# Performance work log

Hardware: AMD Instinct MI355X
Metric: run time of the kernel (lower is better)

Reference implementation:

```python
import jax, jax.numpy as jnp
import numpy as np

B, S, D = 4, 4096, 1024
UNITS = 1024
NRF = 1024


def setup_inputs() -> dict:
    key = jax.random.key(0)
    ks = jax.random.split(key, 10)
    s = 1.0 / np.sqrt(D)
    return {
        "query": jax.random.normal(ks[0], (B, S, D), dtype=jnp.float32),
        "value": jax.random.normal(ks[1], (B, S, D), dtype=jnp.float32),
        "Wq": jax.random.normal(ks[2], (D, UNITS), dtype=jnp.float32) * s,
        "bq": jnp.zeros((UNITS,), dtype=jnp.float32),
        "Wk": jax.random.normal(ks[3], (D, UNITS), dtype=jnp.float32) * s,
        "bk": jnp.zeros((UNITS,), dtype=jnp.float32),
        "Wv": jax.random.normal(ks[4], (D, UNITS), dtype=jnp.float32) * s,
        "bv": jnp.zeros((UNITS,), dtype=jnp.float32),
        # non-trainable random-feature projection (initializer='random_normal', stddev 0.05 in keras)
        "random_weights": jax.random.normal(ks[5], (UNITS, NRF), dtype=jnp.float32) * 0.05,
        "random_bias": jax.random.normal(ks[6], (NRF,), dtype=jnp.float32) * 0.05,
    }


def reference(query, value, Wq, bq, Wk, bk, Wv, bv, random_weights, random_bias):
    # Dense projections: [B,S,D] @ [D,U] -> [B,S,U]
    Q = query @ Wq + bq
    K = value @ Wk + bk
    V = value @ Wv + bv
    # random-feature kernel map: cos(x @ W_r + b_r) -> [B,S,F]
    Q_hat = jnp.cos(Q @ random_weights + random_bias)
    K_hat = jnp.cos(K @ random_weights + random_bias)
    # standard QK^T-softmax-V attention over the feature-mapped Q/K
    scores = jnp.einsum("bqf,bkf->bqk", Q_hat, K_hat)  # [B,S,S]
    probs = jax.nn.softmax(scores, axis=-1)
    return jnp.einsum("bqk,bkd->bqd", probs, V)  # [B,S,U]
```

## Files before the change

### kernel.cpp

```cpp
#include <hip/hip_runtime.h>
#include <hip/hip_bf16.h>
#include <hip/hip_fp16.h>
#include <cstdint>


typedef _Float16 f16;
typedef _Float16 f16x8 __attribute__((ext_vector_type(8)));
typedef _Float16 f16x4 __attribute__((ext_vector_type(4)));
typedef float f32x4 __attribute__((ext_vector_type(4)));

typedef __attribute__((address_space(1))) unsigned int uas1;
typedef __attribute__((address_space(3))) unsigned int uas3;

#define NB 4
#define SEQ 4096
#define DIM 1024

__device__ __forceinline__ void async_copy16(void* lds, const void* g) {
  __builtin_amdgcn_global_load_lds((uas1*)(uintptr_t)g, (uas3*)(uintptr_t)lds,
                                   16, 0, 0);
}


__global__ __launch_bounds__(256) void f2h(const float* __restrict__ in,
                                           f16* __restrict__ out, int n4) {
  int i = blockIdx.x * 256 + threadIdx.x;
  if (i < n4) {
    float4 v = ((const float4*)in)[i];
    f16x4 h = {(f16)v.x, (f16)v.y, (f16)v.z, (f16)v.w};
    ((f16x4*)out)[i] = h;
  }
}

__global__ __launch_bounds__(256) void f2h_split(const float* __restrict__ in,
                                                 f16* __restrict__ hi,
                                                 f16* __restrict__ lo, int n4) {
  int i = blockIdx.x * 256 + threadIdx.x;
  if (i < n4) {
    float4 v = ((const float4*)in)[i];
    f16 h0 = (f16)v.x, h1 = (f16)v.y, h2 = (f16)v.z, h3 = (f16)v.w;
    f16x4 hv = {h0, h1, h2, h3};
    f16x4 lv = {(f16)(v.x - (float)h0), (f16)(v.y - (float)h1),
                (f16)(v.z - (float)h2), (f16)(v.w - (float)h3)};
    ((f16x4*)hi)[i] = hv;
    ((f16x4*)lo)[i] = lv;
  }
}

__global__ __launch_bounds__(256) void f2h_split2(const float* __restrict__ in,
                                                  f16* __restrict__ w2, int n4) {
  int i = blockIdx.x * 256 + threadIdx.x;
  if (i < n4) {
    float4 v = ((const float4*)in)[i];
    f16 h0 = (f16)v.x, h1 = (f16)v.y, h2 = (f16)v.z, h3 = (f16)v.w;
    f16x4 hv = {h0, h1, h2, h3};
    f16x4 lv = {(f16)(v.x - (float)h0), (f16)(v.y - (float)h1),
                (f16)(v.z - (float)h2), (f16)(v.w - (float)h3)};
    const int n = i >> 8, k4 = i & 255;
    ((f16x4*)(w2 + (long)n * 2048))[k4] = hv;
    ((f16x4*)(w2 + (long)n * 2048 + 1024))[k4] = lv;
  }
}

__global__ void tr_h(const f16* __restrict__ in, f16* __restrict__ out, int R,
                     int C) {
  __shared__ f16 tile[32][33];
  int c0 = blockIdx.x * 32, r0 = blockIdx.y * 32;
  tile[threadIdx.y][threadIdx.x] =
      in[(long)(r0 + threadIdx.y) * C + c0 + threadIdx.x];
  __syncthreads();
  out[(long)(c0 + threadIdx.y) * R + r0 + threadIdx.x] =
      tile[threadIdx.x][threadIdx.y];
}

__global__ __launch_bounds__(256) void bias_fold(const float* __restrict__ br,
                                                 const float* __restrict__ bvec,
                                                 const float* __restrict__ Wr,
                                                 float* __restrict__ outb) {
  int f = blockIdx.x * 256 + threadIdx.x;
  float s = br[f];
  for (int u = 0; u < DIM; ++u) s = fmaf(bvec[u], Wr[(long)u * DIM + f], s);
  outb[f] = s;
}

__global__ __launch_bounds__(256) void merge_pair(const float* __restrict__ ml,
                                                  const float* __restrict__ ll,
                                                  f16* __restrict__ scl) {
  int i = blockIdx.x * 256 + threadIdx.x;
  int z2 = i >> 12, row = i & 4095;
  const float* m = ml + z2 * 65536 + row;
  const float* lp = ll + z2 * 65536 + row;
  float a[16];
  float mg = -1e30f;
#pragma unroll 16
  for (int t = 0; t < 16; ++t) mg = fmaxf(mg, m[t * 4096]);
  float l = 0.f;
#pragma unroll 16
  for (int t = 0; t < 16; ++t) {
    a[t] = __expf(m[t * 4096] - mg);
    l += lp[t * 4096] * a[t];
  }
  float li = 1.0f / l;
#pragma unroll 16
  for (int t = 0; t < 16; ++t)
    scl[z2 * 65536 + t * 4096 + row] = (f16)(a[t] * li);
}

__global__ void sentinel(float* out) { out[0] = 12345.0f; }

template <int EPI, int NT, bool WRAPA, int GX>
__global__ __launch_bounds__(512, 2) void g8p(
    const f16* __restrict__ A, const f16* __restrict__ B,
    void* __restrict__ Cv, const float* __restrict__ aux,
    float* __restrict__ mout, float* __restrict__ lout, long sA, long sB,
    long sC, int lda, int ldb, int ldc) {
  constexpr int BUF = 65536;
  __shared__ __align__(16) char smem[2 * BUF];
  __shared__ float red[EPI == 6 ? 4 : 1][EPI == 6 ? 256 : 1];
  int lin = blockIdx.x + blockIdx.y * GX;
  lin = ((lin & 7) << 5) | (lin >> 3);
  const int tn = lin % GX, tm = lin / GX;
  const int z = blockIdx.z;
  const int t = threadIdx.x, w = t >> 6, l = t & 63;
  const int l4 = l >> 4, l15 = l & 15;
  const int wm = w >> 2, wn = w & 3;
  f32x4 acc[8][4] = {};
  const f16* Az = A + (long)z * sA;
  const f16* Bz = B + (long)z * sB;

  auto STAGE_HT = [&](int buf, int tt, int ht) {
    const bool isA = (ht < 2);
    const f16* src = isA ? Az : Bz;
    const int ld = isA ? lda : ldb;
    const int row0 = (isA ? tm : tn) * 256 + (ht & 1) * 128;
    char* base = smem + buf * BUF + (ht >> 1) * 32768 + (ht & 1) * 16384;
    int kk = tt * 64;
    if (WRAPA && isA) kk &= 1023;
#pragma unroll
    for (int j = 0; j < 2; ++j) {
      const int cb = j * 512 + w * 64;
      const int c = cb + l;
      const int r = c >> 3, s = c & 7;
      async_copy16(base + cb * 16,
                   src + (long)(row0 + r) * ld + kk + (s ^ (r & 7)) * 8);
    }
  };

  STAGE_HT(0, 0, 0);
  STAGE_HT(0, 0, 1);
  STAGE_HT(0, 0, 2);
  STAGE_HT(0, 0, 3);
  STAGE_HT(1, 1, 2);
  STAGE_HT(1, 1, 3);
  asm volatile("s_waitcnt vmcnt(4)" ::: "memory");
  __builtin_amdgcn_s_barrier();

  for (int it = 0; it < NT / 2; ++it) {
    const int tt = 2 * it;
    const bool more = (tt + 2) < NT;
    {
      const f16* Ab = (const f16*)(smem);
      const f16* Bb = Ab + 16384;
      f16x8 bfp[4][2];
#pragma unroll
      for (int q = 0; q < 4; ++q) {
        if (q == 0) {
#pragma unroll
          for (int jn = 0; jn < 4; ++jn)
#pragma unroll
            for (int ks = 0; ks < 2; ++ks) {
              const int rb = wn * 64 + jn * 16 + l15;
              const int p = ks * 4 + l4;
              bfp[jn][ks] = *(const f16x8*)&Bb[rb * 64 + (p ^ (rb & 7)) * 8];
            }
        }
        f16x8 af[2][2];
#pragma unroll
        for (int i2 = 0; i2 < 2; ++i2)
#pragma unroll
          for (int ks = 0; ks < 2; ++ks) {
            const int ra = wm * 128 + (q * 2 + i2) * 16 + l15;
            const int p = ks * 4 + l4;
            af[i2][ks] = *(const f16x8*)&Ab[ra * 64 + (p ^ (ra & 7)) * 8];
          }
        if (q == 0) STAGE_HT(1, tt + 1, 0);
        if (q == 1) STAGE_HT(1, tt + 1, 1);
        if (q == 2 && more) STAGE_HT(0, tt + 2, 2);
        if (q == 3) {
          if (more) {
            STAGE_HT(0, tt + 2, 3);
            asm volatile("s_waitcnt vmcnt(4)" ::: "memory");
          } else {
            asm volatile("s_waitcnt vmcnt(0)" ::: "memory");
          }
        }
        __builtin_amdgcn_s_barrier();
        asm volatile("s_waitcnt lgkmcnt(0)" ::: "memory");
        __builtin_amdgcn_s_setprio(1);
#pragma unroll
        for (int i2 = 0; i2 < 2; ++i2)
#pragma unroll
          for (int jn = 0; jn < 4; ++jn)
#pragma unroll
            for (int ks = 0; ks < 2; ++ks)
              acc[q * 2 + i2][jn] = __builtin_amdgcn_mfma_f32_16x16x32_f16(
                  af[i2][ks], bfp[jn][ks], acc[q * 2 + i2][jn], 0, 0, 0);
        __builtin_amdgcn_s_setprio(0);
        __builtin_amdgcn_s_barrier();
      }
    }
    {
      const f16* Ab = (const f16*)(smem + BUF);
      const f16* Bb = Ab + 16384;
      f16x8 bfp[4][2];
#pragma unroll
      for (int q = 0; q < 4; ++q) {
        if (q == 0) {
#pragma unroll
          for (int jn = 0; jn < 4; ++jn)
#pragma unroll
            for (int ks = 0; ks < 2; ++ks) {
              const int rb = wn * 64 + jn * 16 + l15;
              const int p = ks * 4 + l4;
              bfp[jn][ks] = *(const f16x8*)&Bb[rb * 64 + (p ^ (rb & 7)) * 8];
            }
        }
        f16x8 af[2][2];
#pragma unroll
        for (int i2 = 0; i2 < 2; ++i2)
#pragma unroll
          for (int ks = 0; ks < 2; ++ks) {
            const int ra = wm * 128 + (q * 2 + i2) * 16 + l15;
            const int p = ks * 4 + l4;
            af[i2][ks] = *(const f16x8*)&Ab[ra * 64 + (p ^ (ra & 7)) * 8];
          }
        if (q == 0 && more) STAGE_HT(0, tt + 2, 0);
        if (q == 1 && more) STAGE_HT(0, tt + 2, 1);
        if (q == 2 && more) STAGE_HT(1, tt + 3, 2);
        if (q == 3) {
          if (more) {
            STAGE_HT(1, tt + 3, 3);
            asm volatile("s_waitcnt vmcnt(4)" ::: "memory");
          } else {
            asm volatile("s_waitcnt vmcnt(0)" ::: "memory");
          }
        }
        __builtin_amdgcn_s_barrier();
        asm volatile("s_waitcnt lgkmcnt(0)" ::: "memory");
        __builtin_amdgcn_s_setprio(1);
#pragma unroll
        for (int i2 = 0; i2 < 2; ++i2)
#pragma unroll
          for (int jn = 0; jn < 4; ++jn)
#pragma unroll
            for (int ks = 0; ks < 2; ++ks)
              acc[q * 2 + i2][jn] = __builtin_amdgcn_mfma_f32_16x16x32_f16(
                  af[i2][ks], bfp[jn][ks], acc[q * 2 + i2][jn], 0, 0, 0);
        __builtin_amdgcn_s_setprio(0);
        __builtin_amdgcn_s_barrier();
      }
    }
  }

  if constexpr (EPI == 1) {
#pragma unroll
    for (int i = 0; i < 8; ++i) {
      const int row0 = tm * 256 + wm * 128 + i * 16 + l4 * 4;
#pragma unroll
      for (int jn = 0; jn < 4; ++jn) {
        const int col = tn * 256 + wn * 64 + jn * 16 + l15;
#pragma unroll
        for (int r = 0; r < 4; ++r)
          ((f16*)Cv)[(long)z * sC + (long)(row0 + r) * ldc + col] =
              (f16)__cosf(acc[i][jn][r] + aux[col]);
      }
    }
    return;
  }

  float mrow[32];
#pragma unroll
  for (int i = 0; i < 8; ++i)
#pragma unroll
    for (int r = 0; r < 4; ++r) {
      float v = fmaxf(fmaxf(acc[i][0][r], acc[i][1][r]),
                      fmaxf(acc[i][2][r], acc[i][3][r]));
      v = fmaxf(v, __shfl_xor(v, 1));
      v = fmaxf(v, __shfl_xor(v, 2));
      v = fmaxf(v, __shfl_xor(v, 4));
      v = fmaxf(v, __shfl_xor(v, 8));
      if (l15 == 0) red[wn][wm * 128 + i * 16 + l4 * 4 + r] = v;
    }
  __syncthreads();
#pragma unroll
  for (int i = 0; i < 8; ++i)
#pragma unroll
    for (int r = 0; r < 4; ++r) {
      const int rin = wm * 128 + i * 16 + l4 * 4 + r;
      mrow[i * 4 + r] = fmaxf(fmaxf(red[0][rin], red[1][rin]),
                              fmaxf(red[2][rin], red[3][rin]));
    }
  __syncthreads();
#pragma unroll
  for (int i = 0; i < 8; ++i)
#pragma unroll
    for (int r = 0; r < 4; ++r) {
      const float mn = mrow[i * 4 + r];
      float s = 0.f;
#pragma unroll
      for (int jn = 0; jn < 4; ++jn) {
        float e = __expf(acc[i][jn][r] - mn);
        acc[i][jn][r] = e;
        s += e;
      }
      s += __shfl_xor(s, 1);
      s += __shfl_xor(s, 2);
      s += __shfl_xor(s, 4);
      s += __shfl_xor(s, 8);
      if (l15 == 0) red[wn][wm * 128 + i * 16 + l4 * 4 + r] = s;
    }
  __syncthreads();
  if (wn == 0 && l15 == 0) {
#pragma unroll
    for (int i = 0; i < 8; ++i)
#pragma unroll
      for (int r = 0; r < 4; ++r) {
        const int rin = wm * 128 + i * 16 + l4 * 4 + r;
        const int gidx = z * 65536 + tn * 4096 + tm * 256 + rin;
        mout[gidx] = mrow[i * 4 + r];
        lout[gidx] = red[0][rin] + red[1][rin] + red[2][rin] + red[3][rin];
      }
  }
#pragma unroll
  for (int i = 0; i < 8; ++i) {
    const int row0 = tm * 256 + wm * 128 + i * 16 + l4 * 4;
#pragma unroll
    for (int jn = 0; jn < 4; ++jn) {
      const int col = tn * 256 + wn * 64 + jn * 16 + l15;
#pragma unroll
      for (int r = 0; r < 4; ++r)
        ((f16*)Cv)[(long)z * sC + (long)(row0 + r) * ldc + col] =
            (f16)acc[i][jn][r];
    }
  }
}

template <int EPI, bool DA, bool DB, int BK>
__global__ __launch_bounds__(256) void gemm_bt(
    const f16* __restrict__ Ah, const f16* __restrict__ Al,
    const f16* __restrict__ Bh, const f16* __restrict__ Bl,
    void* __restrict__ Cv, const float* __restrict__ aux,
    const f16* __restrict__ ascl, long sAscl, int M, int N, int K, int lda,
    int ldb, int ldc, long sC, long sA, long sB, int sAux) {
  constexpr int NSTAGE = 2 + (DA ? 1 : 0) + (DB ? 1 : 0);
  constexpr int TILE = 128 * BK * 2;
  constexpr int CPR = BK / 8;
  constexpr int CH = 128 * CPR;
  constexpr int NL = NSTAGE * BK / 16;
  static_assert(NL == 6 || NL == 8, "vmcnt literal");
  constexpr int SCLB = (EPI == 7) ? 4096 : 0;
  __shared__ __align__(16) char smem[2 * NSTAGE * TILE + SCLB];

  const int z = blockIdx.z;
  const int tn = blockIdx.x, tm = blockIdx.y;
  const int t = threadIdx.x, w = t >> 6, l = t & 63;
  const int l4 = l >> 4, l15 = l & 15;
  const int wm = w & 1, wn = w >> 1;
  f32x4 acc[4][4] = {};

  const f16* Az = Ah + (long)z * sA;
  const f16* Bz = Bh + (long)z * sB;
  const f16* Alz = nullptr;
  const f16* Blz = nullptr;
  if constexpr (DA) Alz = Al + (long)z * sA;
  if constexpr (DB) Blz = Bl + (long)z * sB;
  f16* sclLds = (f16*)(smem + 2 * NSTAGE * TILE);

  auto swz = [](int r, int p) -> int {
    if constexpr (BK == 64) return p ^ (r & 7);
    else return p ^ ((r >> 1) & 3);
  };

  auto STAGE = [&](int buf, int kk) {
    char* base = smem + buf * (NSTAGE * TILE);
#pragma unroll
    for (int j = 0; j < CH / 256; ++j) {
      const int cb = j * 256 + w * 64;
      const int c = cb + l;
      const int r = c / CPR, pp = c % CPR;
      const int sc = swz(r, pp);
      const long ra = (long)(tm * 128 + r) * lda + kk + sc * 8;
      const long rb = (long)(tn * 128 + r) * ldb + kk + sc * 8;
      async_copy16(base + cb * 16, Az + ra);
      async_copy16(base + TILE + cb * 16, Bz + rb);
      if constexpr (DA) async_copy16(base + 2 * TILE + cb * 16, Alz + ra);
      if constexpr (DB)
        async_copy16(base + (2 + (DA ? 1 : 0)) * TILE + cb * 16, Blz + rb);
    }
  };

  STAGE(0, 0);
  if constexpr (EPI == 7) {
    const f16* asclz = ascl + (long)z * sAscl;
    const int cb = w * 64;
    const int c = cb + l;
    async_copy16(sclLds + cb * 8,
                 asclz + (long)(c >> 4) * M + tm * 128 + (c & 15) * 8);
  }
  asm volatile("s_waitcnt vmcnt(0)" ::: "memory");
  __syncthreads();

  const int nt = K / BK;
  int cur = 0;
  for (int tt = 0; tt < nt; ++tt) {
    const int kk = tt * BK;
    if (tt + 1 < nt) {
      STAGE(cur ^ 1, kk + BK);
      if constexpr (NL == 6)
        asm volatile("s_waitcnt vmcnt(6)" ::: "memory");
      else
        asm volatile("s_waitcnt vmcnt(8)" ::: "memory");
    } else {
      asm volatile("s_waitcnt vmcnt(0)" ::: "memory");
    }
    __syncthreads();

    const f16* As = (const f16*)(smem + cur * (NSTAGE * TILE));
    const f16* Bs = As + TILE / 2;
    const f16* Als = Bs + TILE / 2;
    const f16* Bls = Als + (DA ? TILE / 2 : 0);

    f16 sA4[4];
    if constexpr (EPI == 7) {
      const int tile = kk >> 8;
#pragma unroll
      for (int i = 0; i < 4; ++i)
        sA4[i] = sclLds[tile * 128 + wm * 64 + i * 16 + l15];
    }

#pragma unroll
    for (int ks = 0; ks < BK / 32; ++ks) {
      f16x8 af[4], bf[4];
#pragma unroll
      for (int i = 0; i < 4; ++i) {
        const int ra = wm * 64 + i * 16 + l15;
        const int rb = wn * 64 + i * 16 + l15;
        af[i] = *(const f16x8*)&As[ra * BK + swz(ra, ks * 4 + l4) * 8];
        bf[i] = *(const f16x8*)&Bs[rb * BK + swz(rb, ks * 4 + l4) * 8];
      }
      if constexpr (EPI == 7) {
#pragma unroll
        for (int i = 0; i < 4; ++i) af[i] = af[i] * sA4[i];
      }
#pragma unroll
      for (int i = 0; i < 4; ++i)
#pragma unroll
        for (int jn = 0; jn < 4; ++jn)
          acc[i][jn] = __builtin_amdgcn_mfma_f32_16x16x32_f16(af[i], bf[jn],
                                                              acc[i][jn], 0, 0, 0);
      if constexpr (DB) {
        f16x8 bl[4];
#pragma unroll
        for (int i = 0; i < 4; ++i) {
          const int rb = wn * 64 + i * 16 + l15;
          bl[i] = *(const f16x8*)&Bls[rb * BK + swz(rb, ks * 4 + l4) * 8];
        }
#pragma unroll
        for (int i = 0; i < 4; ++i)
#pragma unroll
          for (int jn = 0; jn < 4; ++jn)
            acc[i][jn] = __builtin_amdgcn_mfma_f32_16x16x32_f16(
                af[i], bl[jn], acc[i][jn], 0, 0, 0);
      }
      if constexpr (DA) {
        f16x8 al[4];
#pragma unroll
        for (int i = 0; i < 4; ++i) {
          const int ra = wm * 64 + i * 16 + l15;
          al[i] = *(const f16x8*)&Als[ra * BK + swz(ra, ks * 4 + l4) * 8];
        }
#pragma unroll
        for (int i = 0; i < 4; ++i)
#pragma unroll
          for (int jn = 0; jn < 4; ++jn)
            acc[i][jn] = __builtin_amdgcn_mfma_f32_16x16x32_f16(
                al[i], bf[jn], acc[i][jn], 0, 0, 0);
      }
    }
    __syncthreads();
    cur ^= 1;
  }

  const float* auxp = aux + (long)z * sAux;

  if constexpr (EPI == 2) {
    f16* rep = (f16*)smem;
#pragma unroll
    for (int hh = 0; hh < 2; ++hh) {
      __syncthreads();
#pragma unroll
      for (int ii = 0; ii < 2; ++ii) {
        const int i = hh * 2 + ii;
        const int lrow0 = wm * 32 + ii * 16 + l4 * 4;
#pragma unroll
        for (int jn = 0; jn < 4; ++jn) {
          const int col = wn * 64 + jn * 16 + l15;
#pragma unroll
          for (int r = 0; r < 4; ++r) {
            float v = acc[i][jn][r];
            f16 hv = (f16)(v + auxp[tm * 128 + wm * 64 + i * 16 + l4 * 4 + r]);
            rep[(lrow0 + r) * 136 + col] = hv;
          }
        }
      }
      __syncthreads();
#pragma unroll
      for (int pp = 0; pp < 4; ++pp) {
        const int lrow = pp * 16 + (t >> 4);
        const int grow = tm * 128 + (lrow >> 5) * 64 + hh * 32 + (lrow & 31);
        const int gcol = tn * 128 + (t & 15) * 8;
        *(f16x8*)&((f16*)Cv)[(long)z * sC + (long)grow * ldc + gcol] =
            *(const f16x8*)&rep[lrow * 136 + (t & 15) * 8];
      }
    }
  } else {
    float* rep = (float*)smem;
#pragma unroll
    for (int i = 0; i < 4; ++i) {
      __syncthreads();
      const int lrow0 = wm * 16 + l4 * 4;
#pragma unroll
      for (int jn = 0; jn < 4; ++jn) {
        const int col = wn * 64 + jn * 16 + l15;
#pragma unroll
        for (int r = 0; r < 4; ++r) rep[(lrow0 + r) * 132 + col] = acc[i][jn][r];
      }
      __syncthreads();
#pragma unroll
      for (int pp = 0; pp < 4; ++pp) {
        const int lrow = pp * 8 + (t >> 5);
        const int grow = tm * 128 + (lrow >> 4) * 64 + i * 16 + (lrow & 15);
        const int gcol = tn * 128 + (t & 31) * 4;
        *(float4*)&((float*)Cv)[(long)z * sC + (long)grow * ldc + gcol] =
            *(const float4*)&rep[lrow * 132 + (t & 31) * 4];
      }
    }
  }
}


extern "C" void kernel_launch(void* const* d_in, const int* in_sizes, int n_in,
                              void* d_out, int out_size, void* d_ws,
                              size_t ws_size, hipStream_t stream) {
  const float* query = (const float*)d_in[0];
  const float* value = (const float*)d_in[1];
  const float* Wq = (const float*)d_in[2];
  const float* bq = (const float*)d_in[3];
  const float* Wk = (const float*)d_in[4];
  const float* bk = (const float*)d_in[5];
  const float* Wv = (const float*)d_in[6];
  const float* bv = (const float*)d_in[7];
  const float* Wr = (const float*)d_in[8];
  const float* br = (const float*)d_in[9];
  float* out = (float*)d_out;

  if (ws_size < 169000000ull) {
    sentinel<<<1, 1, 0, stream>>>(out);
    return;
  }

  char* p = (char*)d_ws;
  auto alloc = [&](size_t bytes) {
    char* r = p;
    p += (bytes + 255) & ~(size_t)255;
    return r;
  };
  const size_t QV = 16777216ull;
  const size_t WW = 1048576ull;
  char* bufA = alloc(QV * 2);
  char* bufB = alloc(QV * 2);
  char* bufC = alloc(QV * 2);
  char* bufD = alloc(QV * 2);
  f16* q16 = (f16*)bufA;
  f16* Khat = (f16*)bufA;
  f16* v16 = (f16*)bufB;
  f16* probs0 = (f16*)bufB;
  f16* Qhat = (f16*)bufC;
  f16* VT = (f16*)bufD;
  f16* Wq_h = (f16*)alloc(WW * 2);
  f16* Wq_l = (f16*)alloc(WW * 2);
  f16* Wk_h = (f16*)alloc(WW * 2);
  f16* Wk_l = (f16*)alloc(WW * 2);
  f16* Wr_h = (f16*)alloc(WW * 2);
  f16* Wr_l = (f16*)alloc(WW * 2);
  f16* Wv16 = (f16*)alloc(WW * 2);
  f16* WrT_h = (f16*)alloc(WW * 2);
  f16* WrT_l = (f16*)alloc(WW * 2);
  f16* WvT = (f16*)alloc(WW * 2);
  float* Wtmp32 = (float*)alloc(WW * 8);
  f16* WqrT2 = (f16*)alloc(WW * 4);
  f16* WkrT2 = (f16*)alloc(WW * 4);
  float* brq = (float*)alloc(1024 * 4);
  float* brk = (float*)alloc(1024 * 4);
  float* m_loc = (float*)alloc(2 * 16 * 4096 * 4);
  float* l_loc = (float*)alloc(2 * 16 * 4096 * 4);
  f16* scl = (f16*)alloc(2 * 16 * 4096 * 2);
  const long PSTRIDE = 50331648;

  f2h<<<16384, 256, 0, stream>>>(query, q16, 4194304);
  f2h<<<16384, 256, 0, stream>>>(value, v16, 4194304);
  f2h_split<<<1024, 256, 0, stream>>>(Wq, Wq_h, Wq_l, 262144);
  f2h_split<<<1024, 256, 0, stream>>>(Wk, Wk_h, Wk_l, 262144);
  f2h_split<<<1024, 256, 0, stream>>>(Wr, Wr_h, Wr_l, 262144);
  f2h<<<1024, 256, 0, stream>>>(Wv, Wv16, 262144);
  tr_h<<<dim3(32, 32), dim3(32, 32), 0, stream>>>(Wr_h, WrT_h, 1024, 1024);
  tr_h<<<dim3(32, 32), dim3(32, 32), 0, stream>>>(Wr_l, WrT_l, 1024, 1024);
  tr_h<<<dim3(32, 32), dim3(32, 32), 0, stream>>>(Wv16, WvT, 1024, 1024);
  bias_fold<<<4, 256, 0, stream>>>(br, bq, Wr, brq);
  bias_fold<<<4, 256, 0, stream>>>(br, bk, Wr, brk);

  gemm_bt<5, true, true, 32><<<dim3(8, 8, 2), 256, 0, stream>>>(
      WrT_h, WrT_l, Wq_h, Wq_l, Wtmp32, nullptr, nullptr, 0, 1024, 1024, 1024,
      1024, 1024, 1024, 1048576, 0, 2097152, 0);
  f2h_split2<<<1024, 256, 0, stream>>>(Wtmp32, WqrT2, 262144);
  f2h_split2<<<1024, 256, 0, stream>>>(Wtmp32 + 1048576, WkrT2, 262144);

  g8p<1, 32, true, 4><<<dim3(4, 64, 1), 512, 0, stream>>>(
      q16, WqrT2, Qhat, brq, nullptr, nullptr, 0, 0, 0, 1024, 2048, 1024);
  g8p<1, 32, true, 4><<<dim3(4, 64, 1), 512, 0, stream>>>(
      v16, WkrT2, Khat, brk, nullptr, nullptr, 0, 0, 0, 1024, 2048, 1024);
  gemm_bt<2, false, false, 64><<<dim3(128, 8, 1), 256, 0, stream>>>(
      WvT, nullptr, v16, nullptr, VT, bv, nullptr, 0, 1024, 16384, 1024, 1024,
      1024, 16384, 0, 0, 0, 0);

  for (int zb = 0; zb < NB; zb += 2) {
    g8p<6, 16, false, 16><<<dim3(16, 16, 2), 512, 0, stream>>>(
        Qhat + (long)zb * 4194304, Khat + (long)zb * 4194304, probs0, nullptr,
        m_loc, l_loc, 4194304, 4194304, PSTRIDE, 1024, 1024, 4096);
    merge_pair<<<32, 256, 0, stream>>>(m_loc, l_loc, scl);
    gemm_bt<7, false, false, 64><<<dim3(8, 32, 2), 256, 0, stream>>>(
        probs0, nullptr, VT + (long)zb * 4096, nullptr, out + (long)zb * 4194304,
        nullptr, scl, 65536, 4096, 1024, 4096, 4096, 16384, 1024, 4194304,
        PSTRIDE, 4096, 0);
  }
}
```

Measured before the change: 684.9 us.

## Merge small prep kernels, parallelize bias fold, stage g8p epilogue through LDS

Merges the two input fp32-to-fp16 conversions into one launch and the three weight transposes into one launch. Splits the serial 1024-long bias fold into a 16-way partial-sum kernel plus a reduction so it uses more than four blocks. The g8p epilogue now writes its tile into padded LDS and then emits coalesced 16-byte global stores instead of scattered 2-byte stores. The larger LDS array (about 132 KB) may limit how many blocks fit per CU.

```diff
diff --git a/kernel.cpp b/kernel.cpp
--- a/kernel.cpp
+++ b/kernel.cpp
@@ -21,6 +21,19 @@
                                    16, 0, 0);
 }
 
+
+__global__ __launch_bounds__(256) void f2h_qv(const float* __restrict__ a,
+                                              const float* __restrict__ b,
+                                              f16* __restrict__ oa,
+                                              f16* __restrict__ ob) {
+  const int bid = blockIdx.x;
+  const float* in = bid < 16384 ? a : b;
+  f16* out = bid < 16384 ? oa : ob;
+  const int i = (bid & 16383) * 256 + threadIdx.x;
+  float4 v = ((const float4*)in)[i];
+  f16x4 h = {(f16)v.x, (f16)v.y, (f16)v.z, (f16)v.w};
+  ((f16x4*)out)[i] = h;
+}
 
 __global__ __launch_bounds__(256) void f2h(const float* __restrict__ in,
                                            f16* __restrict__ out, int n4) {
@@ -62,24 +75,43 @@
   }
 }
 
-__global__ void tr_h(const f16* __restrict__ in, f16* __restrict__ out, int R,
-                     int C) {
+__global__ void tr3(const f16* __restrict__ i0, f16* __restrict__ o0,
+                    const f16* __restrict__ i1, f16* __restrict__ o1,
+                    const f16* __restrict__ i2, f16* __restrict__ o2) {
   __shared__ f16 tile[32][33];
+  const f16* in = blockIdx.z == 0 ? i0 : blockIdx.z == 1 ? i1 : i2;
+  f16* out = blockIdx.z == 0 ? o0 : blockIdx.z == 1 ? o1 : o2;
   int c0 = blockIdx.x * 32, r0 = blockIdx.y * 32;
   tile[threadIdx.y][threadIdx.x] =
-      in[(long)(r0 + threadIdx.y) * C + c0 + threadIdx.x];
+      in[(long)(r0 + threadIdx.y) * 1024 + c0 + threadIdx.x];
   __syncthreads();
-  out[(long)(c0 + threadIdx.y) * R + r0 + threadIdx.x] =
+  out[(long)(c0 + threadIdx.y) * 1024 + r0 + threadIdx.x] =
       tile[threadIdx.x][threadIdx.y];
 }
 
-__global__ __launch_bounds__(256) void bias_fold(const float* __restrict__ br,
-                                                 const float* __restrict__ bvec,
+__global__ __launch_bounds__(256) void bias_part(const float* __restrict__ bq,
+                                                 const float* __restrict__ bk,
                                                  const float* __restrict__ Wr,
-                                                 float* __restrict__ outb) {
-  int f = blockIdx.x * 256 + threadIdx.x;
+                                                 float* __restrict__ part) {
+  const float* bvec = blockIdx.z ? bk : bq;
+  const int f = blockIdx.x * 256 + threadIdx.x;
+  const int u0 = blockIdx.y * 64;
+  float s = 0.f;
+#pragma unroll 8
+  for (int u = 0; u < 64; ++u)
+    s = fmaf(bvec[u0 + u], Wr[(long)(u0 + u) * DIM + f], s);
+  part[(blockIdx.z * 16 + blockIdx.y) * 1024 + f] = s;
+}
+
+__global__ __launch_bounds__(256) void bias_red(const float* __restrict__ br,
+                                                const float* __restrict__ part,
+                                                float* __restrict__ brq,
+                                                float* __restrict__ brk) {
+  const int f = blockIdx.x * 256 + threadIdx.x;
+  float* outb = blockIdx.z ? brk : brq;
   float s = br[f];
-  for (int u = 0; u < DIM; ++u) s = fmaf(bvec[u], Wr[(long)u * DIM + f], s);
+#pragma unroll 16
+  for (int j = 0; j < 16; ++j) s += part[(blockIdx.z * 16 + j) * 1024 + f];
   outb[f] = s;
 }
 
@@ -115,7 +147,7 @@
     float* __restrict__ mout, float* __restrict__ lout, long sA, long sB,
     long sC, int lda, int ldb, int ldc) {
   constexpr int BUF = 65536;
-  __shared__ __align__(16) char smem[2 * BUF];
+  __shared__ __align__(16) char smem[256 * 264 * 2];
   __shared__ float red[EPI == 6 ? 4 : 1][EPI == 6 ? 256 : 1];
   int lin = blockIdx.x + blockIdx.y * GX;
   lin = ((lin & 7) << 5) | (lin >> 3);
@@ -262,86 +294,88 @@
     }
   }
 
-  if constexpr (EPI == 1) {
-#pragma unroll
-    for (int i = 0; i < 8; ++i) {
-      const int row0 = tm * 256 + wm * 128 + i * 16 + l4 * 4;
-#pragma unroll
-      for (int jn = 0; jn < 4; ++jn) {
-        const int col = tn * 256 + wn * 64 + jn * 16 + l15;
-#pragma unroll
-        for (int r = 0; r < 4; ++r)
-          ((f16*)Cv)[(long)z * sC + (long)(row0 + r) * ldc + col] =
-              (f16)__cosf(acc[i][jn][r] + aux[col]);
-      }
-    }
-    return;
-  }
-
-  float mrow[32];
-#pragma unroll
-  for (int i = 0; i < 8; ++i)
-#pragma unroll
-    for (int r = 0; r < 4; ++r) {
-      float v = fmaxf(fmaxf(acc[i][0][r], acc[i][1][r]),
-                      fmaxf(acc[i][2][r], acc[i][3][r]));
-      v = fmaxf(v, __shfl_xor(v, 1));
-      v = fmaxf(v, __shfl_xor(v, 2));
-      v = fmaxf(v, __shfl_xor(v, 4));
-      v = fmaxf(v, __shfl_xor(v, 8));
-      if (l15 == 0) red[wn][wm * 128 + i * 16 + l4 * 4 + r] = v;
-    }
-  __syncthreads();
-#pragma unroll
-  for (int i = 0; i < 8; ++i)
-#pragma unroll
-    for (int r = 0; r < 4; ++r) {
-      const int rin = wm * 128 + i * 16 + l4 * 4 + r;
-      mrow[i * 4 + r] = fmaxf(fmaxf(red[0][rin], red[1][rin]),
-                              fmaxf(red[2][rin], red[3][rin]));
-    }
-  __syncthreads();
-#pragma unroll
-  for (int i = 0; i < 8; ++i)
-#pragma unroll
-    for (int r = 0; r < 4; ++r) {
-      const float mn = mrow[i * 4 + r];
-      float s = 0.f;
-#pragma unroll
-      for (int jn = 0; jn < 4; ++jn) {
-        float e = __expf(acc[i][jn][r] - mn);
-        acc[i][jn][r] = e;
-        s += e;
-      }
-      s += __shfl_xor(s, 1);
-      s += __shfl_xor(s, 2);
-      s += __shfl_xor(s, 4);
-      s += __shfl_xor(s, 8);
-      if (l15 == 0) red[wn][wm * 128 + i * 16 + l4 * 4 + r] = s;
-    }
-  __syncthreads();
-  if (wn == 0 && l15 == 0) {
+  if constexpr (EPI == 6) {
+    float mrow[32];
+#pragma unroll
+    for (int i = 0; i < 8; ++i)
+#pragma unroll
+      for (int r = 0; r < 4; ++r) {
+        float v = fmaxf(fmaxf(acc[i][0][r], acc[i][1][r]),
+                        fmaxf(acc[i][2][r], acc[i][3][r]));
+        v = fmaxf(v, __shfl_xor(v, 1));
+        v = fmaxf(v, __shfl_xor(v, 2));
+        v = fmaxf(v, __shfl_xor(v, 4));
+        v = fmaxf(v, __shfl_xor(v, 8));
+        if (l15 == 0) red[wn][wm * 128 + i * 16 + l4 * 4 + r] = v;
+      }
+    __syncthreads();
 #pragma unroll
     for (int i = 0; i < 8; ++i)
 #pragma unroll
       for (int r = 0; r < 4; ++r) {
         const int rin = wm * 128 + i * 16 + l4 * 4 + r;
-        const int gidx = z * 65536 + tn * 4096 + tm * 256 + rin;
-        mout[gidx] = mrow[i * 4 + r];
-        lout[gidx] = red[0][rin] + red[1][rin] + red[2][rin] + red[3][rin];
-      }
-  }
+        mrow[i * 4 + r] = fmaxf(fmaxf(red[0][rin], red[1][rin]),
+                                fmaxf(red[2][rin], red[3][rin]));
+      }
+    __syncthreads();
+#pragma unroll
+    for (int i = 0; i < 8; ++i)
+#pragma unroll
+      for (int r = 0; r < 4; ++r) {
+        const float mn = mrow[i * 4 + r];
+        float s = 0.f;
+#pragma unroll
+        for (int jn = 0; jn < 4; ++jn) {
+          float e = __expf(acc[i][jn][r] - mn);
+          acc[i][jn][r] = e;
+          s += e;
+        }
+        s += __shfl_xor(s, 1);
+        s += __shfl_xor(s, 2);
+        s += __shfl_xor(s, 4);
+        s += __shfl_xor(s, 8);
+        if (l15 == 0) red[wn][wm * 128 + i * 16 + l4 * 4 + r] = s;
+      }
+    __syncthreads();
+    if (wn == 0 && l15 == 0) {
+#pragma unroll
+      for (int i = 0; i < 8; ++i)
+#pragma unroll
+        for (int r = 0; r < 4; ++r) {
+          const int rin = wm * 128 + i * 16 + l4 * 4 + r;
+          const int gidx = z * 65536 + tn * 4096 + tm * 256 + rin;
+          mout[gidx] = mrow[i * 4 + r];
+          lout[gidx] = red[0][rin] + red[1][rin] + red[2][rin] + red[3][rin];
+        }
+    }
+  }
+
+  f16* rep = (f16*)smem;
 #pragma unroll
   for (int i = 0; i < 8; ++i) {
-    const int row0 = tm * 256 + wm * 128 + i * 16 + l4 * 4;
+    const int row0 = wm * 128 + i * 16 + l4 * 4;
 #pragma unroll
     for (int jn = 0; jn < 4; ++jn) {
-      const int col = tn * 256 + wn * 64 + jn * 16 + l15;
-#pragma unroll
-      for (int r = 0; r < 4; ++r)
-        ((f16*)Cv)[(long)z * sC + (long)(row0 + r) * ldc + col] =
-            (f16)acc[i][jn][r];
-    }
+      const int col = wn * 64 + jn * 16 + l15;
+#pragma unroll
+      for (int r = 0; r < 4; ++r) {
+        float v = acc[i][jn][r];
+        f16 hv;
+        if constexpr (EPI == 1)
+          hv = (f16)__cosf(v + aux[tn * 256 + col]);
+        else
+          hv = (f16)v;
+        rep[(row0 + r) * 264 + col] = hv;
+      }
+    }
+  }
+  __syncthreads();
+#pragma unroll
+  for (int k = 0; k < 16; ++k) {
+    const int orow = k * 16 + (t >> 5);
+    const int oc = (t & 31) * 8;
+    *(f16x8*)&((f16*)Cv)[(long)z * sC + (long)(tm * 256 + orow) * ldc +
+                         tn * 256 + oc] = *(const f16x8*)&rep[orow * 264 + oc];
   }
 }
 
@@ -602,22 +636,21 @@
   f16* WkrT2 = (f16*)alloc(WW * 4);
   float* brq = (float*)alloc(1024 * 4);
   float* brk = (float*)alloc(1024 * 4);
+  float* bpart = (float*)alloc(2 * 16 * 1024 * 4);
   float* m_loc = (float*)alloc(2 * 16 * 4096 * 4);
   float* l_loc = (float*)alloc(2 * 16 * 4096 * 4);
   f16* scl = (f16*)alloc(2 * 16 * 4096 * 2);
   const long PSTRIDE = 50331648;
 
-  f2h<<<16384, 256, 0, stream>>>(query, q16, 4194304);
-  f2h<<<16384, 256, 0, stream>>>(value, v16, 4194304);
+  f2h_qv<<<32768, 256, 0, stream>>>(query, value, q16, v16);
   f2h_split<<<1024, 256, 0, stream>>>(Wq, Wq_h, Wq_l, 262144);
   f2h_split<<<1024, 256, 0, stream>>>(Wk, Wk_h, Wk_l, 262144);
   f2h_split<<<1024, 256, 0, stream>>>(Wr, Wr_h, Wr_l, 262144);
   f2h<<<1024, 256, 0, stream>>>(Wv, Wv16, 262144);
-  tr_h<<<dim3(32, 32), dim3(32, 32), 0, stream>>>(Wr_h, WrT_h, 1024, 1024);
-  tr_h<<<dim3(32, 32), dim3(32, 32), 0, stream>>>(Wr_l, WrT_l, 1024, 1024);
-  tr_h<<<dim3(32, 32), dim3(32, 32), 0, stream>>>(Wv16, WvT, 1024, 1024);
-  bias_fold<<<4, 256, 0, stream>>>(br, bq, Wr, brq);
-  bias_fold<<<4, 256, 0, stream>>>(br, bk, Wr, brk);
+  tr3<<<dim3(32, 32, 3), dim3(32, 32), 0, stream>>>(Wr_h, WrT_h, Wr_l, WrT_l,
+                                                    Wv16, WvT);
+  bias_part<<<dim3(4, 16, 2), 256, 0, stream>>>(bq, bk, Wr, bpart);
+  bias_red<<<dim3(4, 1, 2), 256, 0, stream>>>(br, bpart, brq, brk);
 
   gemm_bt<5, true, true, 32><<<dim3(8, 8, 2), 256, 0, stream>>>(
       WrT_h, WrT_l, Wq_h, Wq_l, Wtmp32, nullptr, nullptr, 0, 1024, 1024, 1024,
```

After: 621.2 us. 9.3% less time.
